# Kernel tuning notes

Measured on AMD Instinct MI355X. Metric: run time of the kernel, lower is better.

## Reference

```python
import jax, jax.numpy as jnp
import numpy as np

D = 1024          # dim_in == dim_out
H = 16            # num_heads
G = 4             # num_kv_groups
HD = D // H       # head_dim = 64
GS = H // G       # group_size = 4
S = 2048          # context_length / seq_len
B = 2
EPS = 1e-05


def setup_inputs() -> dict:
    key = jax.random.key(0)
    ks = jax.random.split(key, 12)
    sd = 0.02
    return {
        "x":  jax.random.normal(ks[0], (B, S, D), jnp.float32),
        # torch.nn.Linear weights are stored [out_features, in_features]
        "wq": jax.random.normal(ks[1], (D, D), jnp.float32) * sd,
        "wk": jax.random.normal(ks[2], (G * HD, D), jnp.float32) * sd,
        "wv": jax.random.normal(ks[3], (G * HD, D), jnp.float32) * sd,
        "wo": jax.random.normal(ks[4], (D, D), jnp.float32) * sd,
        "w1": jax.random.normal(ks[5], (4 * D, D), jnp.float32) * sd,
        "w2": jax.random.normal(ks[6], (D, 4 * D), jnp.float32) * sd,
        "g1": jnp.ones((D,), jnp.float32),
        "b1": jnp.zeros((D,), jnp.float32),
        "g2": jnp.ones((D,), jnp.float32),
        "b2": jnp.zeros((D,), jnp.float32),
    }


def _layernorm(x, gamma, beta):
    mean = jnp.mean(x, axis=-1, keepdims=True)
    var = jnp.var(x, axis=-1, keepdims=True)  # unbiased=False
    return (x - mean) * jax.lax.rsqrt(var + EPS) * gamma + beta


def _gelu_tanh(x):
    c = jnp.sqrt(jnp.asarray(2.0 / jnp.pi, x.dtype))
    return 0.5 * x * (1.0 + jnp.tanh(c * (x + 0.044715 * x ** 3)))


def _gqa(x, wq, wk, wv, wo):
    b, s, _ = x.shape
    q = (x @ wq.T).reshape(b, s, H, HD).transpose(0, 2, 1, 3)   # [B,H,S,hd]
    k = (x @ wk.T).reshape(b, s, G, HD).transpose(0, 2, 1, 3)   # [B,G,S,hd]
    v = (x @ wv.T).reshape(b, s, G, HD).transpose(0, 2, 1, 3)
    k = jnp.repeat(k, GS, axis=1)                               # [B,H,S,hd]
    v = jnp.repeat(v, GS, axis=1)
    scores = jnp.einsum('bhqd,bhkd->bhqk', q, k)                # [B,H,S,S]
    causal = jnp.tril(jnp.ones((s, s), bool))
    scores = jnp.where(causal, scores, -jnp.inf)
    attn = jax.nn.softmax(scores / jnp.sqrt(jnp.asarray(HD, scores.dtype)), axis=-1)
    ctx = jnp.einsum('bhqk,bhkd->bhqd', attn, v)                # [B,H,S,hd]
    ctx = ctx.transpose(0, 2, 1, 3).reshape(b, s, D)
    return ctx @ wo.T


def reference(x, wq, wk, wv, wo, w1, w2, g1, b1, g2, b2):
    h = x + _gqa(_layernorm(x, g1, b1), wq, wk, wv, wo)
    ff = _layernorm(h, g2, b2) @ w1.T
    ff = _gelu_tanh(ff) @ w2.T
    return h + ff
```

## Files before the change

kernel.cpp:

```cpp
#include <hip/hip_runtime.h>
#include <stdint.h>

typedef __bf16 bf16_t;
typedef bf16_t bf16x8 __attribute__((ext_vector_type(8)));
typedef bf16_t bf16x4 __attribute__((ext_vector_type(4)));
typedef float f32x4 __attribute__((ext_vector_type(4)));

#define DEVFN static __device__ __forceinline__

DEVFN void gload_lds16(const void* g, void* l) {
  __builtin_amdgcn_global_load_lds((const __attribute__((address_space(1))) void*)g,
                                   (__attribute__((address_space(3))) void*)l, 16, 0, 0);
}

DEVFN float gelu_f(float x) {
  float u = 0.7978845608028654f * (x + 0.044715f * x * x * x);
  float e = __expf(2.0f * u);
  float t = 1.0f - 2.0f / (e + 1.0f);
  return 0.5f * x * (1.0f + t);
}

template <int CTRL>
DEVFN float dpp_rot(float x) {
  int i = __builtin_bit_cast(int, x);
  int r = __builtin_amdgcn_update_dpp(i, i, CTRL, 0xF, 0xF, false);
  return __builtin_bit_cast(float, r);
}
DEVFN float dpp_sum16(float x) {
  x += dpp_rot<0x121>(x);
  x += dpp_rot<0x122>(x);
  x += dpp_rot<0x124>(x);
  x += dpp_rot<0x128>(x);
  return x;
}

__global__ void cvt_kernel(const float* __restrict__ s, bf16_t* __restrict__ d, int n4) {
  int i = blockIdx.x * blockDim.x + threadIdx.x;
  int stride = gridDim.x * blockDim.x;
  for (; i < n4; i += stride) {
    float4 v = ((const float4*)s)[i];
    bf16x4 o;
    o[0] = (bf16_t)v.x; o[1] = (bf16_t)v.y; o[2] = (bf16_t)v.z; o[3] = (bf16_t)v.w;
    ((bf16x4*)d)[i] = o;
  }
}

__global__ void cvt4_kernel(const float* __restrict__ wq, const float* __restrict__ wk,
                            const float* __restrict__ wv, const float* __restrict__ wo,
                            bf16_t* __restrict__ qkv_dst, bf16_t* __restrict__ wo_dst) {
  int i = blockIdx.x * blockDim.x + threadIdx.x;
  int stride = gridDim.x * blockDim.x;
  for (; i < 655360; i += stride) {
    const float* s;
    bf16_t* d;
    int j;
    if (i < 262144) { s = wq; d = qkv_dst; j = i; }
    else if (i < 327680) { s = wk; d = qkv_dst + 1048576; j = i - 262144; }
    else if (i < 393216) { s = wv; d = qkv_dst + 1310720; j = i - 327680; }
    else { s = wo; d = wo_dst; j = i - 393216; }
    float4 v = ((const float4*)s)[j];
    bf16x4 o;
    o[0] = (bf16_t)v.x; o[1] = (bf16_t)v.y; o[2] = (bf16_t)v.z; o[3] = (bf16_t)v.w;
    ((bf16x4*)d)[j] = o;
  }
}

__global__ __launch_bounds__(256) void ln_kernel(const float* __restrict__ in,
                                                 const float* __restrict__ gamma,
                                                 const float* __restrict__ beta,
                                                 bf16_t* __restrict__ out) {
  const int row = blockIdx.x;
  const int tid = threadIdx.x;
  const float4 v = ((const float4*)(in + (size_t)row * 1024))[tid];
  float s = v.x + v.y + v.z + v.w;
  float q = v.x * v.x + v.y * v.y + v.z * v.z + v.w * v.w;
#pragma unroll
  for (int off = 1; off < 64; off <<= 1) {
    s += __shfl_xor(s, off);
    q += __shfl_xor(q, off);
  }
  __shared__ float ss[4], qs[4];
  if ((tid & 63) == 0) { ss[tid >> 6] = s; qs[tid >> 6] = q; }
  __syncthreads();
  s = ss[0] + ss[1] + ss[2] + ss[3];
  q = qs[0] + qs[1] + qs[2] + qs[3];
  const float mean = s * (1.0f / 1024.0f);
  const float var = q * (1.0f / 1024.0f) - mean * mean;
  const float rstd = rsqrtf(var + 1e-5f);
  const float4 g4 = ((const float4*)gamma)[tid];
  const float4 b4 = ((const float4*)beta)[tid];
  bf16x4 o;
  o[0] = (bf16_t)((v.x - mean) * rstd * g4.x + b4.x);
  o[1] = (bf16_t)((v.y - mean) * rstd * g4.y + b4.y);
  o[2] = (bf16_t)((v.z - mean) * rstd * g4.z + b4.z);
  o[3] = (bf16_t)((v.w - mean) * rstd * g4.w + b4.w);
  *(bf16x4*)(out + (size_t)row * 1024 + tid * 4) = o;
}

template <int EPI, int BM>
__global__ __launch_bounds__(256, (BM == 64 ? 3 : 2))
void gemm_bt(const bf16_t* __restrict__ A, const bf16_t* __restrict__ W,
             bf16_t* outb, float* outf, const float* resid, int M, int N, int K) {
  constexpr int MI = BM / 32;
  constexpr int WRS = BM / 2;
  __shared__ __align__(16) bf16_t As[2][2][BM * 32];
  __shared__ __align__(16) bf16_t Bs[2][2][128 * 32];
  const int tid = threadIdx.x;
  const int lane = tid & 63;
  const int wid = tid >> 6;
  const int l15 = lane & 15;
  const int l4 = lane >> 4;
  const int m0 = blockIdx.y * BM;
  const int n0 = blockIdx.x * 128;
  const int wr = wid >> 1;
  const int wc = wid & 1;

  const int sr = lane >> 2;
  const int sk = (lane & 3) * 8;
  const bf16_t* aBase;
  if constexpr (BM == 128) aBase = A + (size_t)(m0 + wid * 32 + sr) * K + sk;
  else                     aBase = A + (size_t)(m0 + wid * 16 + sr) * K + sk;
  const bf16_t* bBase = W + (size_t)(n0 + wid * 32 + sr) * K + sk;
  const size_t rowOff16 = (size_t)16 * K;

  f32x4 acc[MI][4] = {};
  const int NT = K / 64;

  auto stage = [&](int buf, int t) {
    const int kt = t * 64;
#pragma unroll
    for (int kk = 0; kk < 2; ++kk) {
      const int ko = kt + kk * 32;
      if constexpr (BM == 128) {
        gload_lds16(aBase + ko, &As[buf][kk][wid * 1024]);
        gload_lds16(aBase + ko + rowOff16, &As[buf][kk][wid * 1024 + 512]);
      } else {
        gload_lds16(aBase + ko, &As[buf][kk][wid * 512]);
      }
      gload_lds16(bBase + ko, &Bs[buf][kk][wid * 1024]);
      gload_lds16(bBase + ko + rowOff16, &Bs[buf][kk][wid * 1024 + 512]);
    }
  };

  stage(0, 0);
  for (int t = 0; t < NT; ++t) {
    __syncthreads();
    if (t + 1 < NT) stage((t + 1) & 1, t + 1);
    const int buf = t & 1;
#pragma unroll
    for (int kk = 0; kk < 2; ++kk) {
      bf16x8 af[MI], bfr[4];
#pragma unroll
      for (int i = 0; i < MI; ++i)
        af[i] = *(const bf16x8*)&As[buf][kk][(wr * WRS + i * 16 + l15) * 32 + l4 * 8];
#pragma unroll
      for (int j = 0; j < 4; ++j)
        bfr[j] = *(const bf16x8*)&Bs[buf][kk][(wc * 64 + j * 16 + l15) * 32 + l4 * 8];
#pragma unroll
      for (int i = 0; i < MI; ++i)
#pragma unroll
        for (int j = 0; j < 4; ++j)
          acc[i][j] = __builtin_amdgcn_mfma_f32_16x16x32_bf16(af[i], bfr[j], acc[i][j], 0, 0, 0);
    }
  }

  const int col0 = n0 + wc * 64 + l15;
  const int row0 = m0 + wr * WRS + l4 * 4;
#pragma unroll
  for (int i = 0; i < MI; ++i) {
#pragma unroll
    for (int r = 0; r < 4; ++r) {
      const size_t row = (size_t)(row0 + i * 16 + r);
#pragma unroll
      for (int j = 0; j < 4; ++j) {
        const size_t idx = row * N + col0 + j * 16;
        const float v = acc[i][j][r];
        if constexpr (EPI == 0) {
          outb[idx] = (bf16_t)v;
        } else if constexpr (EPI == 1) {
          outb[idx] = (bf16_t)gelu_f(v);
        } else {
          outf[idx] = resid[idx] + v;
        }
      }
    }
  }
}

static __device__ const int kQbTab[40] = {0,1,2,3,4,4,5,5,6,6,7,7,8,8,8,9,9,9,10,10,10,
                                          11,11,11,12,12,12,12,13,13,13,13,14,14,14,14,15,15,15,15};
static __device__ const int kCTab[40]  = {0,0,0,0,0,1,0,1,0,1,0,1,0,1,2,0,1,2,0,1,2,
                                          0,1,2,0,1,2,3,0,1,2,3,0,1,2,3,0,1,2,3};
static __device__ const int kPrefix16[16] = {0,1,2,3,4,6,8,10,12,15,18,21,24,28,32,36};

__global__ __launch_bounds__(256, 3) void attn_kernel(const bf16_t* __restrict__ qkv,
                                                      bf16_t* __restrict__ pO,
                                                      float* __restrict__ pML) {
  __shared__ __align__(16) bf16_t Ks[2][64 * 68];
  __shared__ __align__(16) bf16_t Vt[2][64 * 68];
  __shared__ __align__(16) bf16_t Ps[4][32 * 68];
  const int tid = threadIdx.x, lane = tid & 63, wid = tid >> 6;
  const int l15 = lane & 15, l4 = lane >> 4;
  const int bx = blockIdx.x;
  const int qb = kQbTab[bx] * 128;
  const int kv_lo = kCTab[bx] * 512;
  const int kv_hi = min(qb + 128, kv_lo + 512);
  const int h = blockIdx.y, b = blockIdx.z;
  const int g = h >> 2;
  const int slot = (b * 16 + h) * 40 + bx;
  const size_t RS = 1536;
  const bf16_t* qbase = qkv + (size_t)b * 2048 * RS + h * 64;
  const bf16_t* kbase = qkv + (size_t)b * 2048 * RS + 1024 + g * 64;
  const bf16_t* vbase = kbase + 256;
  const float C2S = 0.125f * 1.44269504088896340736f;

  bf16x8 qf[2][2];
#pragma unroll
  for (int rf = 0; rf < 2; ++rf)
#pragma unroll
    for (int kc = 0; kc < 2; ++kc) {
      bf16x8 raw = *(const bf16x8*)(qbase + (size_t)(qb + wid * 32 + rf * 16 + l15) * RS +
                                    kc * 32 + l4 * 8);
#pragma unroll
      for (int e = 0; e < 8; ++e) qf[rf][kc][e] = (bf16_t)((float)raw[e] * C2S);
    }

  f32x4 po[2][4] = {};
  float l_i[2][4] = {};

  const int sKrow = tid >> 2, sKc = (tid & 3) * 16;
  const int sVkey = tid & 63, sVd = (tid >> 6) * 16;
  const bf16_t* kRowPtr = kbase + (size_t)sKrow * RS + sKc;
  const bf16_t* vRowPtr = vbase + (size_t)sVkey * RS + sVd;

  uint4 k0 = *(const uint4*)(kRowPtr + (size_t)kv_lo * RS);
  uint4 k1 = *(const uint4*)(kRowPtr + (size_t)kv_lo * RS + 8);
  bf16x8 v0 = *(const bf16x8*)(vRowPtr + (size_t)kv_lo * RS);
  bf16x8 v1 = *(const bf16x8*)(vRowPtr + (size_t)kv_lo * RS + 8);
  *(uint4*)&Ks[0][sKrow * 68 + sKc] = k0;
  *(uint4*)&Ks[0][sKrow * 68 + sKc + 8] = k1;
#pragma unroll
  for (int i = 0; i < 8; ++i) {
    Vt[0][(sVd + i) * 68 + sVkey] = v0[i];
    Vt[0][(sVd + 8 + i) * 68 + sVkey] = v1[i];
  }

  const int fb0 = qb + wid * 32;
  int cur = 0;
  for (int kv0 = kv_lo; kv0 < kv_hi; kv0 += 64) {
    __syncthreads();
    const bool more = (kv0 + 64) < kv_hi;
    if (more) {
      const bf16_t* kp = kRowPtr + (size_t)(kv0 + 64) * RS;
      const bf16_t* vp = vRowPtr + (size_t)(kv0 + 64) * RS;
      k0 = *(const uint4*)kp;
      k1 = *(const uint4*)(kp + 8);
      v0 = *(const bf16x8*)vp;
      v1 = *(const bf16x8*)(vp + 8);
    }

    f32x4 sAcc[2][4] = {};
#pragma unroll
    for (int jt = 0; jt < 4; ++jt) {
#pragma unroll
      for (int kc = 0; kc < 2; ++kc) {
        bf16x8 kf = *(const bf16x8*)&Ks[cur][(jt * 16 + l15) * 68 + kc * 32 + l4 * 8];
        sAcc[0][jt] = __builtin_amdgcn_mfma_f32_16x16x32_bf16(qf[0][kc], kf, sAcc[0][jt], 0, 0, 0);
        sAcc[1][jt] = __builtin_amdgcn_mfma_f32_16x16x32_bf16(qf[1][kc], kf, sAcc[1][jt], 0, 0, 0);
      }
    }

#pragma unroll
    for (int rf = 0; rf < 2; ++rf) {
      const int fb = fb0 + rf * 16;
      if (kv0 > fb + 15) continue;
      bf16_t* psb = &Ps[wid][(rf * 16 + l4 * 4) * 68 + l15];
      float rsum[4] = {0.f, 0.f, 0.f, 0.f};
      const bool diag = (kv0 + 63 > fb);
#pragma unroll
      for (int jt = 0; jt < 4; ++jt)
#pragma unroll
        for (int r = 0; r < 4; ++r) {
          float sv = sAcc[rf][jt][r];
          if (diag) {
            const int key = kv0 + jt * 16 + l15;
            sv = (key <= fb + l4 * 4 + r) ? sv : -3.0e38f;
          }
          const float e = exp2f(sv);
          rsum[r] += e;
          psb[r * 68 + jt * 16] = (bf16_t)e;
        }
#pragma unroll
      for (int r = 0; r < 4; ++r) l_i[rf][r] += dpp_sum16(rsum[r]);
    }

    if (kv0 <= fb0 + 31) {
      const bool do0 = (kv0 <= fb0 + 15);
#pragma unroll
      for (int kc = 0; kc < 2; ++kc) {
        bf16x8 pa1 = *(const bf16x8*)&Ps[wid][(16 + l15) * 68 + kc * 32 + l4 * 8];
        bf16x8 pa0;
        if (do0) pa0 = *(const bf16x8*)&Ps[wid][l15 * 68 + kc * 32 + l4 * 8];
#pragma unroll
        for (int jd = 0; jd < 4; ++jd) {
          bf16x8 vf = *(const bf16x8*)&Vt[cur][(jd * 16 + l15) * 68 + kc * 32 + l4 * 8];
          if (do0) po[0][jd] = __builtin_amdgcn_mfma_f32_16x16x32_bf16(pa0, vf, po[0][jd], 0, 0, 0);
          po[1][jd] = __builtin_amdgcn_mfma_f32_16x16x32_bf16(pa1, vf, po[1][jd], 0, 0, 0);
        }
      }
    }

    if (more) {
      *(uint4*)&Ks[cur ^ 1][sKrow * 68 + sKc] = k0;
      *(uint4*)&Ks[cur ^ 1][sKrow * 68 + sKc + 8] = k1;
#pragma unroll
      for (int i = 0; i < 8; ++i) {
        Vt[cur ^ 1][(sVd + i) * 68 + sVkey] = v0[i];
        Vt[cur ^ 1][(sVd + 8 + i) * 68 + sVkey] = v1[i];
      }
    }
    cur ^= 1;
  }

#pragma unroll
  for (int rf = 0; rf < 2; ++rf) {
#pragma unroll
    for (int r = 0; r < 4; ++r) {
      const int lrow = wid * 32 + rf * 16 + l4 * 4 + r;
      if (l15 == 0) {
        pML[((size_t)slot * 128 + lrow) * 2] = 0.0f;
        pML[((size_t)slot * 128 + lrow) * 2 + 1] = l_i[rf][r];
      }
#pragma unroll
      for (int jd = 0; jd < 4; ++jd)
        pO[((size_t)slot * 128 + lrow) * 64 + jd * 16 + l15] = (bf16_t)po[rf][jd][r];
    }
  }
}

__global__ __launch_bounds__(256) void attn_combine(const bf16_t* __restrict__ pO,
                                                    const float* __restrict__ pML,
                                                    bf16_t* __restrict__ ctx) {
  const int i = blockIdx.x, h = blockIdx.y, b = blockIdx.z;
  const int C = (i >> 2) + 1;
  const int base = (b * 16 + h) * 40 + kPrefix16[i];
  const int row = threadIdx.x >> 1;
  const int half = (threadIdx.x & 1) * 32;
  float m = -3.0e38f;
  for (int c = 0; c < C; ++c)
    m = fmaxf(m, pML[((size_t)(base + c) * 128 + row) * 2]);
  float L = 0.0f, acc[32];
#pragma unroll
  for (int e = 0; e < 32; ++e) acc[e] = 0.0f;
  for (int c = 0; c < C; ++c) {
    const float mc = pML[((size_t)(base + c) * 128 + row) * 2];
    const float lc = pML[((size_t)(base + c) * 128 + row) * 2 + 1];
    const float w = exp2f(mc - m);
    L += w * lc;
    const bf16_t* op = pO + ((size_t)(base + c) * 128 + row) * 64 + half;
#pragma unroll
    for (int j = 0; j < 4; ++j) {
      bf16x8 v = *(const bf16x8*)(op + j * 8);
#pragma unroll
      for (int e = 0; e < 8; ++e) acc[j * 8 + e] += w * (float)v[e];
    }
  }
  const float inv = 1.0f / L;
  bf16_t* outp = ctx + ((size_t)b * 2048 + i * 128 + row) * 1024 + h * 64 + half;
#pragma unroll
  for (int j = 0; j < 4; ++j) {
    bf16x8 o;
#pragma unroll
    for (int e = 0; e < 8; ++e) o[e] = (bf16_t)(acc[j * 8 + e] * inv);
    *(bf16x8*)(outp + j * 8) = o;
  }
}

extern "C" void kernel_launch(void* const* d_in, const int* in_sizes, int n_in,
                              void* d_out, int out_size, void* d_ws, size_t ws_size,
                              hipStream_t stream) {
  const float* x = (const float*)d_in[0];
  const float* wq = (const float*)d_in[1];
  const float* wk = (const float*)d_in[2];
  const float* wv = (const float*)d_in[3];
  const float* wo = (const float*)d_in[4];
  const float* w1 = (const float*)d_in[5];
  const float* w2 = (const float*)d_in[6];
  const float* g1 = (const float*)d_in[7];
  const float* b1 = (const float*)d_in[8];
  const float* g2 = (const float*)d_in[9];
  const float* b2 = (const float*)d_in[10];
  float* out = (float*)d_out;

  char* ws = (char*)d_ws;
  bf16_t* qkv = (bf16_t*)(ws + 0);
  bf16_t* ctx = (bf16_t*)(ws + 12582912);
  bf16_t* wo_b = (bf16_t*)(ws + 20971520);
  bf16_t* wqkv_b = (bf16_t*)(ws + 23068672);
  bf16_t* h1 = (bf16_t*)(ws + 26214400);
  bf16_t* pO = (bf16_t*)(ws + 23068672);
  float* pML = (float*)(ws + 45088768);
  bf16_t* w1_b = (bf16_t*)(ws + 0);
  bf16_t* w2_b = (bf16_t*)(ws + 8388608);
  bf16_t* h2 = (bf16_t*)(ws + 16777216);
  bf16_t* ff = (bf16_t*)(ws + 25165824);

  auto cvt = [&](const float* s, bf16_t* d, int n) {
    int n4 = n / 4;
    int grid = (n4 + 255) / 256;
    if (grid > 2048) grid = 2048;
    cvt_kernel<<<grid, 256, 0, stream>>>(s, d, n4);
  };
  cvt4_kernel<<<2048, 256, 0, stream>>>(wq, wk, wv, wo, wqkv_b, wo_b);

  ln_kernel<<<4096, 256, 0, stream>>>(x, g1, b1, h1);
  gemm_bt<0, 64><<<dim3(12, 64), 256, 0, stream>>>(h1, wqkv_b, qkv, nullptr, nullptr, 4096, 1536, 1024);
  attn_kernel<<<dim3(40, 16, 2), 256, 0, stream>>>(qkv, pO, pML);
  cvt(w1, w1_b, 4194304);
  attn_combine<<<dim3(16, 16, 2), 256, 0, stream>>>(pO, pML, ctx);
  gemm_bt<2, 64><<<dim3(8, 64), 256, 0, stream>>>(ctx, wo_b, nullptr, out, x, 4096, 1024, 1024);
  cvt(w2, w2_b, 4194304);
  ln_kernel<<<4096, 256, 0, stream>>>(out, g2, b2, h2);
  gemm_bt<1, 128><<<dim3(32, 32), 256, 0, stream>>>(h2, w1_b, ff, nullptr, nullptr, 4096, 4096, 1024);
  gemm_bt<2, 64><<<dim3(8, 64), 256, 0, stream>>>(ff, w2_b, nullptr, out, out, 4096, 1024, 4096);
}
```

Before: 257.5 us.

## Use 4-stage K pipeline with waitcnt, XCD-aware block swizzle, unify GEMM tile

Restructures the GEMM main loop from a double-buffered 64-wide K step into a 4-buffer, 32-wide K-step pipeline that keeps three tiles of loads in flight. Explicit vmcnt waits replace the full syncthreads before each step. Adds a block-index swizzle that gives each of the 8 XCDs a contiguous range of tiles to improve L2 locality. Drops the BM=128 variant, so the FFN1 GEMM now runs with 64-row tiles on a doubled grid. In exchange there are more barriers per unit of K work and more global loads of W for the large GEMM.

```diff
diff --git a/kernel.cpp b/kernel.cpp
--- a/kernel.cpp
+++ b/kernel.cpp
@@ -97,77 +97,74 @@
   *(bf16x4*)(out + (size_t)row * 1024 + tid * 4) = o;
 }
 
-template <int EPI, int BM>
-__global__ __launch_bounds__(256, (BM == 64 ? 3 : 2))
+template <int EPI>
+__global__ __launch_bounds__(256, 3)
 void gemm_bt(const bf16_t* __restrict__ A, const bf16_t* __restrict__ W,
              bf16_t* outb, float* outf, const float* resid, int M, int N, int K) {
-  constexpr int MI = BM / 32;
-  constexpr int WRS = BM / 2;
-  __shared__ __align__(16) bf16_t As[2][2][BM * 32];
-  __shared__ __align__(16) bf16_t Bs[2][2][128 * 32];
+  __shared__ __align__(16) bf16_t As[4][64 * 32];
+  __shared__ __align__(16) bf16_t Bs[4][128 * 32];
   const int tid = threadIdx.x;
   const int lane = tid & 63;
   const int wid = tid >> 6;
   const int l15 = lane & 15;
   const int l4 = lane >> 4;
-  const int m0 = blockIdx.y * BM;
-  const int n0 = blockIdx.x * 128;
+
+  const int nwg = gridDim.x * gridDim.y;
+  const int bid = blockIdx.y * gridDim.x + blockIdx.x;
+  const int cpx = nwg >> 3;
+  const int swz = (bid & 7) * cpx + (bid >> 3);
+  const int m0 = (swz / gridDim.x) * 64;
+  const int n0 = (swz % gridDim.x) * 128;
+
   const int wr = wid >> 1;
   const int wc = wid & 1;
 
   const int sr = lane >> 2;
   const int sk = (lane & 3) * 8;
-  const bf16_t* aBase;
-  if constexpr (BM == 128) aBase = A + (size_t)(m0 + wid * 32 + sr) * K + sk;
-  else                     aBase = A + (size_t)(m0 + wid * 16 + sr) * K + sk;
+  const bf16_t* aBase = A + (size_t)(m0 + wid * 16 + sr) * K + sk;
   const bf16_t* bBase = W + (size_t)(n0 + wid * 32 + sr) * K + sk;
   const size_t rowOff16 = (size_t)16 * K;
 
-  f32x4 acc[MI][4] = {};
-  const int NT = K / 64;
+  f32x4 acc[2][4] = {};
+  const int NT = K / 32;
 
   auto stage = [&](int buf, int t) {
-    const int kt = t * 64;
-#pragma unroll
-    for (int kk = 0; kk < 2; ++kk) {
-      const int ko = kt + kk * 32;
-      if constexpr (BM == 128) {
-        gload_lds16(aBase + ko, &As[buf][kk][wid * 1024]);
-        gload_lds16(aBase + ko + rowOff16, &As[buf][kk][wid * 1024 + 512]);
-      } else {
-        gload_lds16(aBase + ko, &As[buf][kk][wid * 512]);
-      }
-      gload_lds16(bBase + ko, &Bs[buf][kk][wid * 1024]);
-      gload_lds16(bBase + ko + rowOff16, &Bs[buf][kk][wid * 1024 + 512]);
-    }
+    const int ko = t * 32;
+    gload_lds16(aBase + ko, &As[buf][wid * 512]);
+    gload_lds16(bBase + ko, &Bs[buf][wid * 1024]);
+    gload_lds16(bBase + ko + rowOff16, &Bs[buf][wid * 1024 + 512]);
   };
 
   stage(0, 0);
+  if (NT > 1) stage(1, 1);
+  if (NT > 2) stage(2, 2);
+
   for (int t = 0; t < NT; ++t) {
-    __syncthreads();
-    if (t + 1 < NT) stage((t + 1) & 1, t + 1);
-    const int buf = t & 1;
-#pragma unroll
-    for (int kk = 0; kk < 2; ++kk) {
-      bf16x8 af[MI], bfr[4];
-#pragma unroll
-      for (int i = 0; i < MI; ++i)
-        af[i] = *(const bf16x8*)&As[buf][kk][(wr * WRS + i * 16 + l15) * 32 + l4 * 8];
+    if (t + 2 < NT)      __builtin_amdgcn_s_waitcnt(0xF76);
+    else if (t + 1 < NT) __builtin_amdgcn_s_waitcnt(0xF73);
+    else                 __builtin_amdgcn_s_waitcnt(0xF70);
+    __builtin_amdgcn_s_barrier();
+    __builtin_amdgcn_sched_barrier(0);
+    if (t + 3 < NT) stage((t + 3) & 3, t + 3);
+    const int buf = t & 3;
+    bf16x8 af[2], bfr[4];
+#pragma unroll
+    for (int i = 0; i < 2; ++i)
+      af[i] = *(const bf16x8*)&As[buf][(wr * 32 + i * 16 + l15) * 32 + l4 * 8];
+#pragma unroll
+    for (int j = 0; j < 4; ++j)
+      bfr[j] = *(const bf16x8*)&Bs[buf][(wc * 64 + j * 16 + l15) * 32 + l4 * 8];
+#pragma unroll
+    for (int i = 0; i < 2; ++i)
 #pragma unroll
       for (int j = 0; j < 4; ++j)
-        bfr[j] = *(const bf16x8*)&Bs[buf][kk][(wc * 64 + j * 16 + l15) * 32 + l4 * 8];
-#pragma unroll
-      for (int i = 0; i < MI; ++i)
-#pragma unroll
-        for (int j = 0; j < 4; ++j)
-          acc[i][j] = __builtin_amdgcn_mfma_f32_16x16x32_bf16(af[i], bfr[j], acc[i][j], 0, 0, 0);
-    }
+        acc[i][j] = __builtin_amdgcn_mfma_f32_16x16x32_bf16(af[i], bfr[j], acc[i][j], 0, 0, 0);
   }
 
   const int col0 = n0 + wc * 64 + l15;
-  const int row0 = m0 + wr * WRS + l4 * 4;
-#pragma unroll
-  for (int i = 0; i < MI; ++i) {
+  const int row0 = m0 + wr * 32 + l4 * 4;
+#pragma unroll
+  for (int i = 0; i < 2; ++i) {
 #pragma unroll
     for (int r = 0; r < 4; ++r) {
       const size_t row = (size_t)(row0 + i * 16 + r);
@@ -414,13 +411,13 @@
   cvt4_kernel<<<2048, 256, 0, stream>>>(wq, wk, wv, wo, wqkv_b, wo_b);
 
   ln_kernel<<<4096, 256, 0, stream>>>(x, g1, b1, h1);
-  gemm_bt<0, 64><<<dim3(12, 64), 256, 0, stream>>>(h1, wqkv_b, qkv, nullptr, nullptr, 4096, 1536, 1024);
+  gemm_bt<0><<<dim3(12, 64), 256, 0, stream>>>(h1, wqkv_b, qkv, nullptr, nullptr, 4096, 1536, 1024);
   attn_kernel<<<dim3(40, 16, 2), 256, 0, stream>>>(qkv, pO, pML);
   cvt(w1, w1_b, 4194304);
   attn_combine<<<dim3(16, 16, 2), 256, 0, stream>>>(pO, pML, ctx);
-  gemm_bt<2, 64><<<dim3(8, 64), 256, 0, stream>>>(ctx, wo_b, nullptr, out, x, 4096, 1024, 1024);
+  gemm_bt<2><<<dim3(8, 64), 256, 0, stream>>>(ctx, wo_b, nullptr, out, x, 4096, 1024, 1024);
   cvt(w2, w2_b, 4194304);
   ln_kernel<<<4096, 256, 0, stream>>>(out, g2, b2, h2);
-  gemm_bt<1, 128><<<dim3(32, 32), 256, 0, stream>>>(h2, w1_b, ff, nullptr, nullptr, 4096, 4096, 1024);
-  gemm_bt<2, 64><<<dim3(8, 64), 256, 0, stream>>>(ff, w2_b, nullptr, out, out, 4096, 1024, 4096);
-}
+  gemm_bt<1><<<dim3(32, 64), 256, 0, stream>>>(h2, w1_b, ff, nullptr, nullptr, 4096, 4096, 1024);
+  gemm_bt<2><<<dim3(8, 64), 256, 0, stream>>>(ff, w2_b, nullptr, out, out, 4096, 1024, 4096);
+}
```

Measured after the change: 283.1 us. 9.9% more time.
